# Kernel tuning notes

Hardware: AMD Instinct MI355X
Metric: run time of the kernel (lower is better)

The kernel has to match this reference:

```python
import jax, jax.numpy as jnp
import numpy as np

EPS = 1e-5

def conv(x, w, b=None, padding=0, groups=1, dilation=1):
    out = jax.lax.conv_general_dilated(
        x, w, window_strides=(1, 1), padding=[(padding, padding)] * 2,
        rhs_dilation=(dilation, dilation), feature_group_count=groups,
        dimension_numbers=('NCHW', 'OIHW', 'NCHW'))
    if b is not None:
        out = out + b[None, :, None, None]
    return out

def bn(x, g, b):
    # eval-mode BatchNorm with running_mean=0, running_var=1
    return x * (g / jnp.sqrt(1.0 + EPS))[None, :, None, None] + b[None, :, None, None]

def _gather_bilinear_corner(xf, yi, xi, H, W):
    # xf: [B, C, H*W]; yi/xi: [B, K2, H, W] int32 corner coords
    valid = (yi >= 0) & (yi < H) & (xi >= 0) & (xi < W)
    idx = jnp.clip(yi, 0, H - 1) * W + jnp.clip(xi, 0, W - 1)  # [B,K2,H,W]
    B = xf.shape[0]
    g = jax.vmap(lambda xb, ib: xb[:, ib])(xf, idx.reshape(B, -1))  # [B,C,K2*H*W]
    g = g.reshape(B, xf.shape[1], *yi.shape[1:])  # [B,C,K2,H,W]
    return g * valid[:, None].astype(xf.dtype)

def deform_dw_conv(x, offset, w_dw, pad, dil, kh=3, kw=3):
    # torchvision DeformConv2d, depthwise (groups=C), stride 1.
    # offset: [B, 2*kh*kw, H, W], ordering (dy, dx) per kernel tap.
    B, C, H, W = x.shape
    K2 = kh * kw
    off = offset.reshape(B, K2, 2, H, W)
    dy, dx = off[:, :, 0], off[:, :, 1]  # [B,K2,H,W]
    k = jnp.arange(K2)
    ky = ((k // kw) * dil - pad).astype(x.dtype)  # [K2]
    kx = ((k % kw) * dil - pad).astype(x.dtype)
    py = jnp.arange(H, dtype=x.dtype)[None, None, :, None] + ky[None, :, None, None] + dy
    px = jnp.arange(W, dtype=x.dtype)[None, None, None, :] + kx[None, :, None, None] + dx
    y0 = jnp.floor(py); x0 = jnp.floor(px)
    fy = py - y0; fx = px - x0
    y0i = y0.astype(jnp.int32); x0i = x0.astype(jnp.int32)
    y1i = y0i + 1; x1i = x0i + 1
    xf = x.reshape(B, C, H * W)
    v00 = _gather_bilinear_corner(xf, y0i, x0i, H, W)
    v01 = _gather_bilinear_corner(xf, y0i, x1i, H, W)
    v10 = _gather_bilinear_corner(xf, y1i, x0i, H, W)
    v11 = _gather_bilinear_corner(xf, y1i, x1i, H, W)
    fy = fy[:, None]; fx = fx[:, None]  # [B,1,K2,H,W]
    val = (v00 * (1 - fy) * (1 - fx) + v01 * (1 - fy) * fx
           + v10 * fy * (1 - fx) + v11 * fy * fx)  # [B,C,K2,H,W]
    return jnp.einsum('bckhw,ck->bchw', val, w_dw.reshape(C, K2))

def reference(x, w_conv1, g1, b1, w_off, b_off, w_dw, g_b, b_b,
              w_conv2, g2, b2, w_fc1, b_fc1, w_fc2, b_fc2):
    silu = jax.nn.silu
    h = silu(bn(conv(x, w_conv1), g1, b1))
    # MFC_Bottleneck (n=1): offset conv -> deform depthwise conv -> BN -> SiLU -> residual
    off = conv(h, w_off, b_off, padding=1)
    d = deform_dw_conv(h, off, w_dw, pad=1, dil=1)
    h = silu(bn(d, g_b, b_b)) + h
    y = silu(bn(conv(h, w_conv2), g2, b2))
    # SE block
    s = jnp.mean(y, axis=(2, 3), keepdims=True)
    s = silu(conv(s, w_fc1, b_fc1))
    s = jax.nn.sigmoid(conv(s, w_fc2, b_fc2))
    return y * s

def setup_inputs() -> dict:
    key = jax.random.key(0)
    ks = jax.random.split(key, 8)
    B, C1, C2, HID, H, W = 4, 512, 512, 256, 64, 64
    SQ = C2 // 16
    sc = 0.02
    return {
        'x': jax.random.normal(ks[0], (B, C1, H, W), jnp.float32),
        'w_conv1': jax.random.normal(ks[1], (HID, C1, 1, 1), jnp.float32) * sc,
        'g1': jnp.ones((HID,), jnp.float32),
        'b1': jnp.zeros((HID,), jnp.float32),
        'w_off': jax.random.normal(ks[2], (18, HID, 3, 3), jnp.float32) * sc,
        'b_off': jnp.zeros((18,), jnp.float32),
        'w_dw': jax.random.normal(ks[3], (HID, 1, 3, 3), jnp.float32) * sc,
        'g_b': jnp.ones((HID,), jnp.float32),
        'b_b': jnp.zeros((HID,), jnp.float32),
        'w_conv2': jax.random.normal(ks[4], (C2, HID, 1, 1), jnp.float32) * sc,
        'g2': jnp.ones((C2,), jnp.float32),
        'b2': jnp.zeros((C2,), jnp.float32),
        'w_fc1': jax.random.normal(ks[5], (SQ, C2, 1, 1), jnp.float32) * sc,
        'b_fc1': jnp.zeros((SQ,), jnp.float32),
        'w_fc2': jax.random.normal(ks[6], (C2, SQ, 1, 1), jnp.float32) * sc,
        'b_fc2': jnp.zeros((C2,), jnp.float32),
    }
```

## Files before the change

### kernel.cpp

```cpp
#include <hip/hip_runtime.h>

#define HW 4096
#define BN_RS 0.9999950000374998f

typedef __attribute__((ext_vector_type(8))) short  short8;
typedef __attribute__((ext_vector_type(8))) unsigned short ushort8;
typedef __attribute__((ext_vector_type(4))) float  f32x4;
typedef __attribute__((ext_vector_type(2), aligned(4))) float f32x2u;
typedef __attribute__((ext_vector_type(2), aligned(8))) float f32x2a;

__device__ __forceinline__ float silu_f(float v) { return v / (1.0f + __expf(-v)); }
__device__ __forceinline__ int clamp64(int v) { return v < 0 ? 0 : (v > 63 ? 63 : v); }
__device__ __forceinline__ unsigned short f2bf(float f) {
    union { float f; unsigned u; } v; v.f = f;
    unsigned r = v.u + 0x7fff + ((v.u >> 16) & 1);
    return (unsigned short)(r >> 16);
}
__device__ __forceinline__ unsigned packbf(float lo, float hi) {
    return (unsigned)f2bf(lo) | ((unsigned)f2bf(hi) << 16);
}

template<int CO, int CIN>
__global__ __launch_bounds__(256) void k_conv1x1_mfma(
    const float* __restrict__ X, const float* __restrict__ Wt,
    const float* __restrict__ gg, const float* __restrict__ bb,
    float* __restrict__ Y)
{
    constexpr int NC = CO / 64;
    const int id   = blockIdx.x;
    const int low3 = id & 7;
    const int rest = id >> 3;
    const int c0i  = rest % NC;
    const int tile = (rest / NC) * 8 + low3;
    const int b  = tile >> 6;
    const int p0 = (tile & 63) * 64;
    const int c0 = c0i * 64;

    const int tid  = threadIdx.x;
    const int wave = tid >> 6, lane = tid & 63;
    const int wm = wave >> 1, wn = wave & 1;
    const int lrow = lane & 15, lkg = lane >> 4;

    __shared__ __align__(16) unsigned short As[64 * 40];
    __shared__ __align__(16) unsigned short Bs[64 * 40];

    const float* Xb = X + (size_t)b * CIN * HW;

    f32x4 acc[2][2];
    #pragma unroll
    for (int i = 0; i < 2; ++i)
        #pragma unroll
        for (int j = 0; j < 2; ++j) acc[i][j] = (f32x4){0.f, 0.f, 0.f, 0.f};

    const int arow = tid >> 2, akc = (tid & 3) * 8;
    const int kp = tid >> 4, p4 = (tid & 15) * 4;

    ushort8 aP;
    uint4   bP;

    auto LOAD = [&](int k0) {
        const float* wp = &Wt[(size_t)(c0 + arow) * CIN + k0 + akc];
        float4 v0 = *(const float4*)wp;
        float4 v1 = *(const float4*)(wp + 4);
        ushort8 u;
        u[0] = f2bf(v0.x); u[1] = f2bf(v0.y); u[2] = f2bf(v0.z); u[3] = f2bf(v0.w);
        u[4] = f2bf(v1.x); u[5] = f2bf(v1.y); u[6] = f2bf(v1.z); u[7] = f2bf(v1.w);
        aP = u;
        const float* xp = &Xb[(size_t)(k0 + 2 * kp) * HW + p0 + p4];
        float4 x0 = *(const float4*)xp;
        float4 x1 = *(const float4*)(xp + HW);
        bP.x = packbf(x0.x, x1.x);
        bP.y = packbf(x0.y, x1.y);
        bP.z = packbf(x0.z, x1.z);
        bP.w = packbf(x0.w, x1.w);
    };

    LOAD(0);
    for (int k0 = 0; k0 < CIN; k0 += 32) {
        __syncthreads();
        *(ushort8*)&As[arow * 40 + akc] = aP;
        {
            const int kg = kp >> 2, kl2 = (kp & 3) * 2;
            const unsigned bw[4] = {bP.x, bP.y, bP.z, bP.w};
            #pragma unroll
            for (int jj = 0; jj < 4; ++jj) {
                int pos = p4 + jj;
                int kgs = kg ^ ((pos >> 3) & 3);
                *(unsigned*)&Bs[pos * 40 + kgs * 8 + kl2] = bw[jj];
            }
        }
        __syncthreads();
        if (k0 + 32 < CIN) LOAD(k0 + 32);

        short8 aF[2], bF[2];
        #pragma unroll
        for (int mi = 0; mi < 2; ++mi)
            aF[mi] = *(const short8*)&As[(wm * 32 + mi * 16 + lrow) * 40 + lkg * 8];
        #pragma unroll
        for (int ni = 0; ni < 2; ++ni) {
            int pos = wn * 32 + ni * 16 + lrow;
            int kgs = lkg ^ ((pos >> 3) & 3);
            bF[ni] = *(const short8*)&Bs[pos * 40 + kgs * 8];
        }
        #pragma unroll
        for (int mi = 0; mi < 2; ++mi)
            #pragma unroll
            for (int ni = 0; ni < 2; ++ni)
                acc[mi][ni] = __builtin_amdgcn_mfma_f32_16x16x32_bf16(
                    aF[mi], bF[ni], acc[mi][ni], 0, 0, 0);
    }

    #pragma unroll
    for (int mi = 0; mi < 2; ++mi) {
        #pragma unroll
        for (int r = 0; r < 4; ++r) {
            int co = c0 + wm * 32 + mi * 16 + lkg * 4 + r;
            float s  = gg[co] * BN_RS;
            float bi = bb[co];
            size_t rowb = ((size_t)b * CO + co) * HW + p0 + wn * 32 + lrow;
            Y[rowb]      = silu_f(fmaf(acc[mi][0][r], s, bi));
            Y[rowb + 16] = silu_f(fmaf(acc[mi][1][r], s, bi));
        }
    }
}

__global__ __launch_bounds__(256) void k_woff_t(
    const float* __restrict__ Wo, unsigned short* __restrict__ Wt2)
{
    const int t = blockIdx.x;
    const int co = blockIdx.y;
    const int ci = threadIdx.x;
    float v = (co < 18) ? Wo[((size_t)co * 256 + ci) * 9 + t] : 0.0f;
    Wt2[((size_t)t * 32 + co) * 256 + ci] = f2bf(v);
}

__global__ __launch_bounds__(256) void k_conv_off(
    const float* __restrict__ Hh, const unsigned short* __restrict__ Wt2,
    float* __restrict__ OffP)
{
    const int y = blockIdx.x;
    const int b = blockIdx.y;
    const int q = blockIdx.z;
    const int tid = threadIdx.x;
    const int wn = tid >> 6;
    const int lane = tid & 63;
    const int lrow = lane & 15, lkg = lane >> 4;

    __shared__ __align__(16) unsigned short hsT[3][66][40];

    f32x4 acc[2];
    acc[0] = (f32x4){0.f, 0.f, 0.f, 0.f};
    acc[1] = (f32x4){0.f, 0.f, 0.f, 0.f};

    for (int cc = 0; cc < 2; ++cc) {
        const int ci0 = q * 64 + cc * 32;
        __syncthreads();
        if (tid < 192) {
            int r = tid / 64, which = (tid >> 5) & 1, ci = tid & 31;
            hsT[r][which ? 65 : 0][ci] = 0;
        }
        #pragma unroll
        for (int it = 0; it < 6; ++it) {
            int i  = tid + it * 256;
            int r  = i >> 9;
            int ci = (i >> 4) & 31;
            int x4 = (i & 15) << 2;
            int yy = y + r - 1;
            float4 v = make_float4(0.f, 0.f, 0.f, 0.f);
            if ((unsigned)yy < 64u)
                v = *(const float4*)&Hh[((size_t)(b * 256 + ci0 + ci) << 12) + yy * 64 + x4];
            hsT[r][1 + x4 + 0][ci] = f2bf(v.x);
            hsT[r][1 + x4 + 1][ci] = f2bf(v.y);
            hsT[r][1 + x4 + 2][ci] = f2bf(v.z);
            hsT[r][1 + x4 + 3][ci] = f2bf(v.w);
        }
        __syncthreads();

        #pragma unroll
        for (int t9 = 0; t9 < 9; ++t9) {
            const int ty = t9 / 3, tx = t9 % 3;
            short8 bF = *(const short8*)&hsT[ty][wn * 16 + lrow + tx][lkg * 8];
            #pragma unroll
            for (int mi = 0; mi < 2; ++mi) {
                short8 aF = *(const short8*)&Wt2[((size_t)t9 * 32 + mi * 16 + lrow) * 256
                                                 + ci0 + lkg * 8];
                acc[mi] = __builtin_amdgcn_mfma_f32_16x16x32_bf16(aF, bF, acc[mi], 0, 0, 0);
            }
        }
    }

    #pragma unroll
    for (int mi = 0; mi < 2; ++mi) {
        #pragma unroll
        for (int r = 0; r < 4; ++r) {
            int co = mi * 16 + lkg * 4 + r;
            if (co < 18)
                OffP[(((size_t)q * 4 + b) * 18 + co) * HW + y * 64 + wn * 16 + lrow]
                    = acc[mi][r];
        }
    }
}

__global__ __launch_bounds__(256) void k_off_combine(
    const float* __restrict__ OffP, const float* __restrict__ Bo,
    float* __restrict__ Off2)
{
    const int bk = blockIdx.x;
    const int b = bk / 9, k = bk - b * 9;
    const int t0 = 2 * k, t1 = 2 * k + 1;
    const float bias0 = Bo[t0], bias1 = Bo[t1];
    const size_t p0 = ((size_t)b * 18 + t0) * HW;
    const size_t p1 = ((size_t)b * 18 + t1) * HW;
    float* outp = Off2 + (((size_t)b * 9 + k) * HW) * 2;
    #pragma unroll
    for (int it = 0; it < 4; ++it) {
        int p4 = (threadIdx.x + it * 256) * 4;
        float4 s0 = *(const float4*)&OffP[p0 + p4];
        float4 s1 = *(const float4*)&OffP[p1 + p4];
        #pragma unroll
        for (int q = 1; q < 4; ++q) {
            float4 v0 = *(const float4*)&OffP[((size_t)q * 4 * 18) * HW + p0 + p4];
            float4 v1 = *(const float4*)&OffP[((size_t)q * 4 * 18) * HW + p1 + p4];
            s0.x += v0.x; s0.y += v0.y; s0.z += v0.z; s0.w += v0.w;
            s1.x += v1.x; s1.y += v1.y; s1.z += v1.z; s1.w += v1.w;
        }
        s0.x += bias0; s0.y += bias0; s0.z += bias0; s0.w += bias0;
        s1.x += bias1; s1.y += bias1; s1.z += bias1; s1.w += bias1;
        float4 o01 = make_float4(s0.x, s1.x, s0.y, s1.y);
        float4 o23 = make_float4(s0.z, s1.z, s0.w, s1.w);
        *(float4*)&outp[p4 * 2]     = o01;
        *(float4*)&outp[p4 * 2 + 4] = o23;
    }
}

__global__ __launch_bounds__(256) void k_deform(
    const float* __restrict__ Hh, const float* __restrict__ Off2,
    const float* __restrict__ Wd, const float* __restrict__ Gb,
    const float* __restrict__ Bb, float* __restrict__ H2)
{
    const int idx = blockIdx.x;
    const int bq  = idx & 31;
    const int y   = idx >> 5;
    const int b   = bq >> 3;
    const int q   = bq & 7;
    const int tid = threadIdx.x;
    const int x = tid & 63;
    const int g = tid >> 6;
    const int pos = y * 64 + x;

    __shared__ __align__(16) float hsw[5][32][68];
    __shared__ __align__(16) float wds[9 * 32];
    __shared__ float gbs[32], bbs[32];

    for (int i = tid; i < 288; i += 256) {
        int lc = i & 31, k = i >> 5;
        wds[i] = Wd[(q * 32 + lc) * 9 + k];
    }
    if (tid < 32) {
        gbs[tid] = Gb[q * 32 + tid] * BN_RS;
        bbs[tid] = Bb[q * 32 + tid];
    }

    int w0 = y - 2; w0 = w0 < 0 ? 0 : (w0 > 59 ? 59 : w0);
    const float* hq = Hh + ((size_t)(b * 256 + q * 32) << 12);
    #pragma unroll
    for (int it = 0; it < 10; ++it) {
        int i = tid + it * 256;
        int slot = i >> 9, ch = (i >> 4) & 31, x4 = (i & 15) << 2;
        float4 v = *(const float4*)&hq[((size_t)ch << 12) + (w0 + slot) * 64 + x4];
        *(float4*)&hsw[slot][ch][x4] = v;
    }
    __syncthreads();

    float acc[8];
    #pragma unroll
    for (int j = 0; j < 8; ++j) acc[j] = 0.f;

    const float* Ob   = Off2 + ((size_t)b * 9 * HW + pos) * 2;
    const float* hb0  = hq + ((size_t)(g * 8) << 12);
    const float* ldsb = &hsw[0][0][0];

    for (int r = 0; r < 3; ++r) {
        int   rb0[3], rb1[3], lb0[3], lb1[3];
        float wa0[3], wb0[3], wa1[3], wb1[3];
        bool inw = true;
        #pragma unroll
        for (int t = 0; t < 3; ++t) {
            int k = r * 3 + t;
            f32x2a dv = *(const f32x2a*)(Ob + (size_t)k * HW * 2);
            float dy = dv.x, dx = dv.y;
            float py = (float)(y + r - 1) + dy;
            float px = (float)(x + t - 1) + dx;
            float fy0 = floorf(py), fx0 = floorf(px);
            int y0 = (int)fy0, x0 = (int)fx0;
            float fy = py - fy0, fx = px - fx0;
            bool vy0 = ((unsigned)y0 < 64u), vy1 = ((unsigned)(y0 + 1) < 64u);
            bool vx0 = ((unsigned)x0 < 64u), vx1 = ((unsigned)(x0 + 1) < 64u);
            int cy0 = clamp64(y0), cy1 = clamp64(y0 + 1);
            int bx  = x0 < 0 ? 0 : (x0 > 62 ? 62 : x0);
            int d0 = x0 - bx;
            bool o0 = d0 > 0;
            bool o1 = d0 >= 0;
            rb0[t] = cy0 * 64 + bx;
            rb1[t] = cy1 * 64 + bx;
            lb0[t] = (cy0 - w0) * 2176 + bx;
            lb1[t] = (cy1 - w0) * 2176 + bx;
            inw = inw && (cy0 >= w0) && (cy1 <= w0 + 4);
            float wy0 = vy0 ? (1.0f - fy) : 0.0f;
            float wy1 = vy1 ? fy : 0.0f;
            float wx0 = vx0 ? (1.0f - fx) : 0.0f;
            float wx1 = vx1 ? fx : 0.0f;
            float wa = (o0 ? 0.0f : wx0) + (o1 ? 0.0f : wx1);
            float wb = (o0 ? wx0 : 0.0f) + (o1 ? wx1 : 0.0f);
            wa0[t] = wa * wy0; wb0[t] = wb * wy0;
            wa1[t] = wa * wy1; wb1[t] = wb * wy1;
        }
        if (__all(inw)) {
            #pragma unroll
            for (int j = 0; j < 8; ++j) {
                const int chb = (g * 8 + j) * 68;
                float a = acc[j];
                #pragma unroll
                for (int t = 0; t < 3; ++t) {
                    f32x2u u0 = *(const f32x2u*)(ldsb + lb0[t] + chb);
                    f32x2u u1 = *(const f32x2u*)(ldsb + lb1[t] + chb);
                    float val = u0.x * wa0[t] + u0.y * wb0[t]
                              + u1.x * wa1[t] + u1.y * wb1[t];
                    a = fmaf(val, wds[(r * 3 + t) * 32 + g * 8 + j], a);
                }
                acc[j] = a;
            }
        } else {
            #pragma unroll
            for (int j = 0; j < 8; ++j) {
                const float* hb = hb0 + ((size_t)j << 12);
                float a = acc[j];
                #pragma unroll
                for (int t = 0; t < 3; ++t) {
                    f32x2u u0 = *(const f32x2u*)(hb + rb0[t]);
                    f32x2u u1 = *(const f32x2u*)(hb + rb1[t]);
                    float val = u0.x * wa0[t] + u0.y * wb0[t]
                              + u1.x * wa1[t] + u1.y * wb1[t];
                    a = fmaf(val, wds[(r * 3 + t) * 32 + g * 8 + j], a);
                }
                acc[j] = a;
            }
        }
    }

    const int ry = (y - w0) * 2176 + x;
    #pragma unroll
    for (int j = 0; j < 8; ++j) {
        int lc = g * 8 + j;
        float t = fmaf(acc[j], gbs[lc], bbs[lc]);
        float res = ldsb[ry + lc * 68];
        __builtin_nontemporal_store(silu_f(t) + res,
            &H2[((size_t)(b * 256 + q * 32 + lc) << 12) + pos]);
    }
}

__global__ __launch_bounds__(256) void k_se_reduce(
    const float* __restrict__ Y, float* __restrict__ sb)
{
    const int bc = blockIdx.x;
    const float4* p = (const float4*)(Y + (size_t)bc * HW);
    int tid = threadIdx.x;
    float s = 0.f;
    #pragma unroll
    for (int it = 0; it < 4; ++it) {
        float4 v = p[tid + it * 256];
        s += v.x + v.y + v.z + v.w;
    }
    #pragma unroll
    for (int o = 32; o > 0; o >>= 1) s += __shfl_down(s, o);
    __shared__ float red[4];
    if ((tid & 63) == 0) red[tid >> 6] = s;
    __syncthreads();
    if (tid == 0) sb[bc] = (red[0] + red[1] + red[2] + red[3]) * (1.0f / 4096.0f);
}

__global__ __launch_bounds__(256) void k_se_fc(
    const float* __restrict__ sb, const float* __restrict__ wf1,
    const float* __restrict__ bf1, const float* __restrict__ wf2,
    const float* __restrict__ bf2, float* __restrict__ s2)
{
    const int b = blockIdx.x;
    const int t = threadIdx.x;
    __shared__ float sv[512];
    __shared__ float s1[32];
    sv[t]       = sb[b * 512 + t];
    sv[t + 256] = sb[b * 512 + t + 256];
    __syncthreads();
    if (t < 32) {
        float a = bf1[t];
        const float* w = wf1 + t * 512;
        for (int i = 0; i < 512; ++i) a = fmaf(w[i], sv[i], a);
        s1[t] = silu_f(a);
    }
    __syncthreads();
    #pragma unroll
    for (int it = 0; it < 2; ++it) {
        int co = t + it * 256;
        float a = bf2[co];
        const float* w = wf2 + co * 32;
        #pragma unroll
        for (int i = 0; i < 32; ++i) a = fmaf(w[i], s1[i], a);
        s2[b * 512 + co] = 1.0f / (1.0f + __expf(-a));
    }
}

__global__ __launch_bounds__(256) void k_se_scale(
    float* __restrict__ Y, const float* __restrict__ s2)
{
    size_t i = (size_t)blockIdx.x * 256 + threadIdx.x;
    int bc = (int)(i >> 10);
    float sc = s2[bc];
    float4 v = ((float4*)Y)[i];
    v.x *= sc; v.y *= sc; v.z *= sc; v.w *= sc;
    ((float4*)Y)[i] = v;
}

extern "C" void kernel_launch(void* const* d_in, const int* in_sizes, int n_in,
                              void* d_out, int out_size, void* d_ws, size_t ws_size,
                              hipStream_t stream)
{
    const float* x   = (const float*)d_in[0];
    const float* w1  = (const float*)d_in[1];
    const float* g1  = (const float*)d_in[2];
    const float* b1  = (const float*)d_in[3];
    const float* wof = (const float*)d_in[4];
    const float* bof = (const float*)d_in[5];
    const float* wdw = (const float*)d_in[6];
    const float* gb  = (const float*)d_in[7];
    const float* bbv = (const float*)d_in[8];
    const float* w2  = (const float*)d_in[9];
    const float* g2  = (const float*)d_in[10];
    const float* b2  = (const float*)d_in[11];
    const float* wf1 = (const float*)d_in[12];
    const float* bf1 = (const float*)d_in[13];
    const float* wf2 = (const float*)d_in[14];
    const float* bf2 = (const float*)d_in[15];
    float* out = (float*)d_out;

    const size_t n_h    = 4ull * 256 * HW;
    const size_t n_offp = 4ull * 4 * 18 * HW;
    const size_t n_off  = 4ull * 18 * HW;
    const size_t n_wt2  = 9 * 32 * 256 / 2;
    float* ws = (float*)d_ws;
    float *h, *offp, *offc, *h2, *sb, *s2, *wt2f;
    size_t need = (2 * n_h + n_offp + n_off + 2048 + 2048 + n_wt2 + 1024) * sizeof(float);
    if (ws_size >= need) {
        h = ws; offp = h + n_h; offc = offp + n_offp; h2 = offc + n_off;
        sb = h2 + n_h; s2 = sb + 2048; wt2f = s2 + 2048;
    } else {
        h = out;
        offp = ws; offc = offp + n_offp; h2 = offc + n_off;
        sb = h2 + n_h; s2 = sb + 2048; wt2f = s2 + 2048;
    }
    unsigned short* wt2 = (unsigned short*)wt2f;

    k_conv1x1_mfma<256, 512><<<1024, 256, 0, stream>>>(x, w1, g1, b1, h);
    k_woff_t<<<dim3(9, 32), 256, 0, stream>>>(wof, wt2);
    k_conv_off<<<dim3(64, 4, 4), 256, 0, stream>>>(h, wt2, offp);
    k_off_combine<<<36, 256, 0, stream>>>(offp, bof, offc);
    k_deform<<<2048, 256, 0, stream>>>(h, offc, wdw, gb, bbv, h2);
    k_conv1x1_mfma<512, 256><<<2048, 256, 0, stream>>>(h2, w2, g2, b2, out);
    k_se_reduce<<<2048, 256, 0, stream>>>(out, sb);
    k_se_fc<<<4, 256, 0, stream>>>(sb, wf1, bf1, wf2, bf2, s2);
    k_se_scale<<<8192, 256, 0, stream>>>(out, s2);
}
```

Baseline: 133.7 us.

## Fuse SE average-pool into conv2 epilogue and halve conv1 pixel tile

The second 1x1 conv epilogue now reduces its SiLU outputs per channel across lanes and writes partial sums to a buffer, so the separate SE reduce kernel and its full re-read of the output are removed. The SE FC kernel sums 128 partials per channel itself. The first 1x1 conv also moves to a 32-pixel tile with twice as many blocks, which raises parallelism but halves reuse of the weight tile. The extra shuffles and the serial 128-step partial sum in a 4-block kernel add some cost.

Result: slower. 144.6 us (+8.1%).

```diff
diff --git a/kernel.cpp b/kernel.cpp
--- a/kernel.cpp
+++ b/kernel.cpp
@@ -20,20 +20,24 @@
     return (unsigned)f2bf(lo) | ((unsigned)f2bf(hi) << 16);
 }
 
-template<int CO, int CIN>
+template<int CO, int CIN, int PT, bool SE>
 __global__ __launch_bounds__(256) void k_conv1x1_mfma(
     const float* __restrict__ X, const float* __restrict__ Wt,
     const float* __restrict__ gg, const float* __restrict__ bb,
-    float* __restrict__ Y)
+    float* __restrict__ Y, float* __restrict__ pbuf)
 {
     constexpr int NC = CO / 64;
+    constexpr int PTILES = HW / PT;
+    constexpr int NI = PT / 32;
+
     const int id   = blockIdx.x;
     const int low3 = id & 7;
     const int rest = id >> 3;
     const int c0i  = rest % NC;
     const int tile = (rest / NC) * 8 + low3;
-    const int b  = tile >> 6;
-    const int p0 = (tile & 63) * 64;
+    const int b  = tile / PTILES;
+    const int pt = tile - b * PTILES;
+    const int p0 = pt * PT;
     const int c0 = c0i * 64;
 
     const int tid  = threadIdx.x;
@@ -42,21 +46,22 @@
     const int lrow = lane & 15, lkg = lane >> 4;
 
     __shared__ __align__(16) unsigned short As[64 * 40];
-    __shared__ __align__(16) unsigned short Bs[64 * 40];
+    __shared__ __align__(16) unsigned short Bs[PT * 40];
 
     const float* Xb = X + (size_t)b * CIN * HW;
 
-    f32x4 acc[2][2];
+    f32x4 acc[2][NI];
     #pragma unroll
     for (int i = 0; i < 2; ++i)
         #pragma unroll
-        for (int j = 0; j < 2; ++j) acc[i][j] = (f32x4){0.f, 0.f, 0.f, 0.f};
+        for (int j = 0; j < NI; ++j) acc[i][j] = (f32x4){0.f, 0.f, 0.f, 0.f};
 
     const int arow = tid >> 2, akc = (tid & 3) * 8;
-    const int kp = tid >> 4, p4 = (tid & 15) * 4;
+    const int kp = tid >> 4;
 
     ushort8 aP;
-    uint4   bP;
+    uint4   bP4;
+    uint2   bP2;
 
     auto LOAD = [&](int k0) {
         const float* wp = &Wt[(size_t)(c0 + arow) * CIN + k0 + akc];
@@ -66,13 +71,23 @@
         u[0] = f2bf(v0.x); u[1] = f2bf(v0.y); u[2] = f2bf(v0.z); u[3] = f2bf(v0.w);
         u[4] = f2bf(v1.x); u[5] = f2bf(v1.y); u[6] = f2bf(v1.z); u[7] = f2bf(v1.w);
         aP = u;
-        const float* xp = &Xb[(size_t)(k0 + 2 * kp) * HW + p0 + p4];
-        float4 x0 = *(const float4*)xp;
-        float4 x1 = *(const float4*)(xp + HW);
-        bP.x = packbf(x0.x, x1.x);
-        bP.y = packbf(x0.y, x1.y);
-        bP.z = packbf(x0.z, x1.z);
-        bP.w = packbf(x0.w, x1.w);
+        if constexpr (PT == 64) {
+            const int p4 = (tid & 15) * 4;
+            const float* xp = &Xb[(size_t)(k0 + 2 * kp) * HW + p0 + p4];
+            float4 x0 = *(const float4*)xp;
+            float4 x1 = *(const float4*)(xp + HW);
+            bP4.x = packbf(x0.x, x1.x);
+            bP4.y = packbf(x0.y, x1.y);
+            bP4.z = packbf(x0.z, x1.z);
+            bP4.w = packbf(x0.w, x1.w);
+        } else {
+            const int p2 = (tid & 15) * 2;
+            const float* xp = &Xb[(size_t)(k0 + 2 * kp) * HW + p0 + p2];
+            f32x2a x0 = *(const f32x2a*)xp;
+            f32x2a x1 = *(const f32x2a*)(xp + HW);
+            bP2.x = packbf(x0.x, x1.x);
+            bP2.y = packbf(x0.y, x1.y);
+        }
     };
 
     LOAD(0);
@@ -81,31 +96,43 @@
         *(ushort8*)&As[arow * 40 + akc] = aP;
         {
             const int kg = kp >> 2, kl2 = (kp & 3) * 2;
-            const unsigned bw[4] = {bP.x, bP.y, bP.z, bP.w};
-            #pragma unroll
-            for (int jj = 0; jj < 4; ++jj) {
-                int pos = p4 + jj;
-                int kgs = kg ^ ((pos >> 3) & 3);
-                *(unsigned*)&Bs[pos * 40 + kgs * 8 + kl2] = bw[jj];
+            if constexpr (PT == 64) {
+                const int p4 = (tid & 15) * 4;
+                const unsigned bw[4] = {bP4.x, bP4.y, bP4.z, bP4.w};
+                #pragma unroll
+                for (int jj = 0; jj < 4; ++jj) {
+                    int pos = p4 + jj;
+                    int kgs = kg ^ ((pos >> 3) & 3);
+                    *(unsigned*)&Bs[pos * 40 + kgs * 8 + kl2] = bw[jj];
+                }
+            } else {
+                const int p2 = (tid & 15) * 2;
+                const unsigned bw[2] = {bP2.x, bP2.y};
+                #pragma unroll
+                for (int jj = 0; jj < 2; ++jj) {
+                    int pos = p2 + jj;
+                    int kgs = kg ^ ((pos >> 3) & 3);
+                    *(unsigned*)&Bs[pos * 40 + kgs * 8 + kl2] = bw[jj];
+                }
             }
         }
         __syncthreads();
         if (k0 + 32 < CIN) LOAD(k0 + 32);
 
-        short8 aF[2], bF[2];
+        short8 aF[2], bF[NI];
         #pragma unroll
         for (int mi = 0; mi < 2; ++mi)
             aF[mi] = *(const short8*)&As[(wm * 32 + mi * 16 + lrow) * 40 + lkg * 8];
         #pragma unroll
-        for (int ni = 0; ni < 2; ++ni) {
-            int pos = wn * 32 + ni * 16 + lrow;
+        for (int ni = 0; ni < NI; ++ni) {
+            int pos = wn * (PT / 2) + ni * 16 + lrow;
             int kgs = lkg ^ ((pos >> 3) & 3);
             bF[ni] = *(const short8*)&Bs[pos * 40 + kgs * 8];
         }
         #pragma unroll
         for (int mi = 0; mi < 2; ++mi)
             #pragma unroll
-            for (int ni = 0; ni < 2; ++ni)
+            for (int ni = 0; ni < NI; ++ni)
                 acc[mi][ni] = __builtin_amdgcn_mfma_f32_16x16x32_bf16(
                     aF[mi], bF[ni], acc[mi][ni], 0, 0, 0);
     }
@@ -117,9 +144,22 @@
             int co = c0 + wm * 32 + mi * 16 + lkg * 4 + r;
             float s  = gg[co] * BN_RS;
             float bi = bb[co];
-            size_t rowb = ((size_t)b * CO + co) * HW + p0 + wn * 32 + lrow;
-            Y[rowb]      = silu_f(fmaf(acc[mi][0][r], s, bi));
-            Y[rowb + 16] = silu_f(fmaf(acc[mi][1][r], s, bi));
+            size_t rowb = ((size_t)b * CO + co) * HW + p0 + wn * (PT / 2) + lrow;
+            float vs = 0.f;
+            #pragma unroll
+            for (int ni = 0; ni < NI; ++ni) {
+                float v = silu_f(fmaf(acc[mi][ni][r], s, bi));
+                Y[rowb + ni * 16] = v;
+                vs += v;
+            }
+            if (SE) {
+                vs += __shfl_xor(vs, 1);
+                vs += __shfl_xor(vs, 2);
+                vs += __shfl_xor(vs, 4);
+                vs += __shfl_xor(vs, 8);
+                if (lrow == 0)
+                    pbuf[(size_t)(pt * 2 + wn) * (4 * CO) + b * CO + co] = vs;
+            }
         }
     }
 }
@@ -359,28 +399,8 @@
     }
 }
 
-__global__ __launch_bounds__(256) void k_se_reduce(
-    const float* __restrict__ Y, float* __restrict__ sb)
-{
-    const int bc = blockIdx.x;
-    const float4* p = (const float4*)(Y + (size_t)bc * HW);
-    int tid = threadIdx.x;
-    float s = 0.f;
-    #pragma unroll
-    for (int it = 0; it < 4; ++it) {
-        float4 v = p[tid + it * 256];
-        s += v.x + v.y + v.z + v.w;
-    }
-    #pragma unroll
-    for (int o = 32; o > 0; o >>= 1) s += __shfl_down(s, o);
-    __shared__ float red[4];
-    if ((tid & 63) == 0) red[tid >> 6] = s;
-    __syncthreads();
-    if (tid == 0) sb[bc] = (red[0] + red[1] + red[2] + red[3]) * (1.0f / 4096.0f);
-}
-
 __global__ __launch_bounds__(256) void k_se_fc(
-    const float* __restrict__ sb, const float* __restrict__ wf1,
+    const float* __restrict__ pbuf, const float* __restrict__ wf1,
     const float* __restrict__ bf1, const float* __restrict__ wf2,
     const float* __restrict__ bf2, float* __restrict__ s2)
 {
@@ -388,8 +408,14 @@
     const int t = threadIdx.x;
     __shared__ float sv[512];
     __shared__ float s1[32];
-    sv[t]       = sb[b * 512 + t];
-    sv[t + 256] = sb[b * 512 + t + 256];
+    float a0 = 0.f, a1 = 0.f;
+    for (int s = 0; s < 128; ++s) {
+        const float* p = pbuf + (size_t)s * 2048 + b * 512;
+        a0 += p[t];
+        a1 += p[t + 256];
+    }
+    sv[t]       = a0 * (1.0f / 4096.0f);
+    sv[t + 256] = a1 * (1.0f / 4096.0f);
     __syncthreads();
     if (t < 32) {
         float a = bf1[t];
@@ -445,27 +471,27 @@
     const size_t n_h    = 4ull * 256 * HW;
     const size_t n_offp = 4ull * 4 * 18 * HW;
     const size_t n_off  = 4ull * 18 * HW;
+    const size_t n_pb   = 128ull * 4 * 512;
     const size_t n_wt2  = 9 * 32 * 256 / 2;
     float* ws = (float*)d_ws;
-    float *h, *offp, *offc, *h2, *sb, *s2, *wt2f;
-    size_t need = (2 * n_h + n_offp + n_off + 2048 + 2048 + n_wt2 + 1024) * sizeof(float);
+    float *h, *offp, *offc, *h2, *pb, *s2, *wt2f;
+    size_t need = (2 * n_h + n_offp + n_off + n_pb + 2048 + n_wt2 + 1024) * sizeof(float);
     if (ws_size >= need) {
         h = ws; offp = h + n_h; offc = offp + n_offp; h2 = offc + n_off;
-        sb = h2 + n_h; s2 = sb + 2048; wt2f = s2 + 2048;
+        pb = h2 + n_h; s2 = pb + n_pb; wt2f = s2 + 2048;
     } else {
         h = out;
         offp = ws; offc = offp + n_offp; h2 = offc + n_off;
-        sb = h2 + n_h; s2 = sb + 2048; wt2f = s2 + 2048;
+        pb = h2 + n_h; s2 = pb + n_pb; wt2f = s2 + 2048;
     }
     unsigned short* wt2 = (unsigned short*)wt2f;
 
-    k_conv1x1_mfma<256, 512><<<1024, 256, 0, stream>>>(x, w1, g1, b1, h);
+    k_conv1x1_mfma<256, 512, 32, false><<<2048, 256, 0, stream>>>(x, w1, g1, b1, h, nullptr);
     k_woff_t<<<dim3(9, 32), 256, 0, stream>>>(wof, wt2);
     k_conv_off<<<dim3(64, 4, 4), 256, 0, stream>>>(h, wt2, offp);
     k_off_combine<<<36, 256, 0, stream>>>(offp, bof, offc);
     k_deform<<<2048, 256, 0, stream>>>(h, offc, wdw, gb, bbv, h2);
-    k_conv1x1_mfma<512, 256><<<2048, 256, 0, stream>>>(h2, w2, g2, b2, out);
-    k_se_reduce<<<2048, 256, 0, stream>>>(out, sb);
-    k_se_fc<<<4, 256, 0, stream>>>(sb, wf1, bf1, wf2, bf2, s2);
+    k_conv1x1_mfma<512, 256, 64, true><<<2048, 256, 0, stream>>>(h2, w2, g2, b2, out, pb);
+    k_se_fc<<<4, 256, 0, stream>>>(pb, wf1, bf1, wf2, bf2, s2);
     k_se_scale<<<8192, 256, 0, stream>>>(out, s2);
 }
```

## Pre-transpose input to bf16 pixel-major and feed conv1 MFMA directly from global

Applied to the files above, without the earlier changes.

Adds a kernel that converts the input x to bf16 in a pixel-major (transposed) layout and another that converts conv1 weights to bf16. A new conv1 kernel then loads MFMA operands straight from global memory as contiguous 8-element vectors, with no LDS staging. The aim is to remove the conversion and transpose work from the GEMM inner loop. The cost is an extra pass over the 32 MB input (read fp32, write bf16), two more launches, and extra workspace.

New measurement: 160.7 us. +20.2%, slower.

```diff
diff --git a/kernel.cpp b/kernel.cpp
--- a/kernel.cpp
+++ b/kernel.cpp
@@ -5,6 +5,7 @@
 
 typedef __attribute__((ext_vector_type(8))) short  short8;
 typedef __attribute__((ext_vector_type(8))) unsigned short ushort8;
+typedef __attribute__((ext_vector_type(4))) unsigned short ushort4v;
 typedef __attribute__((ext_vector_type(4))) float  f32x4;
 typedef __attribute__((ext_vector_type(2), aligned(4))) float f32x2u;
 typedef __attribute__((ext_vector_type(2), aligned(8))) float f32x2a;
@@ -18,6 +19,103 @@
 }
 __device__ __forceinline__ unsigned packbf(float lo, float hi) {
     return (unsigned)f2bf(lo) | ((unsigned)f2bf(hi) << 16);
+}
+
+__global__ __launch_bounds__(256) void k_xt(
+    const float* __restrict__ X, unsigned short* __restrict__ Xt)
+{
+    const int p0  = blockIdx.x * 64;
+    const int ci0 = blockIdx.y * 64;
+    const int b   = blockIdx.z;
+    const int tid = threadIdx.x;
+    __shared__ float ld[64][65];
+    #pragma unroll
+    for (int it = 0; it < 4; ++it) {
+        int i = tid + it * 256;
+        int ci = i >> 4, c4 = (i & 15) * 4;
+        float4 v = *(const float4*)&X[((size_t)(b * 512 + ci0 + ci) << 12) + p0 + c4];
+        ld[ci][c4] = v.x; ld[ci][c4 + 1] = v.y; ld[ci][c4 + 2] = v.z; ld[ci][c4 + 3] = v.w;
+    }
+    __syncthreads();
+    #pragma unroll
+    for (int it = 0; it < 4; ++it) {
+        int i = tid + it * 256;
+        int pr = i >> 4, oc4 = (i & 15) * 4;
+        ushort4v u;
+        u[0] = f2bf(ld[oc4 + 0][pr]);
+        u[1] = f2bf(ld[oc4 + 1][pr]);
+        u[2] = f2bf(ld[oc4 + 2][pr]);
+        u[3] = f2bf(ld[oc4 + 3][pr]);
+        *(ushort4v*)&Xt[((size_t)(b << 12) + p0 + pr) * 512 + ci0 + oc4] = u;
+    }
+}
+
+__global__ __launch_bounds__(256) void k_w1b(
+    const float* __restrict__ W, unsigned short* __restrict__ Wb)
+{
+    size_t i = ((size_t)blockIdx.x * 256 + threadIdx.x) * 4;
+    float4 v = *(const float4*)&W[i];
+    ushort4v u;
+    u[0] = f2bf(v.x); u[1] = f2bf(v.y); u[2] = f2bf(v.z); u[3] = f2bf(v.w);
+    *(ushort4v*)&Wb[i] = u;
+}
+
+template<int CO, int CIN>
+__global__ __launch_bounds__(256) void k_conv1_td(
+    const unsigned short* __restrict__ Xt, const unsigned short* __restrict__ Wb,
+    const float* __restrict__ gg, const float* __restrict__ bb,
+    float* __restrict__ Y)
+{
+    constexpr int NC = CO / 64;
+    const int id   = blockIdx.x;
+    const int low3 = id & 7;
+    const int rest = id >> 3;
+    const int c0i  = rest % NC;
+    const int tile = (rest / NC) * 8 + low3;
+    const int b  = tile >> 6;
+    const int p0 = (tile & 63) * 64;
+    const int c0 = c0i * 64;
+
+    const int tid  = threadIdx.x;
+    const int wave = tid >> 6, lane = tid & 63;
+    const int wm = wave >> 1, wn = wave & 1;
+    const int lrow = lane & 15, lkg = lane >> 4;
+
+    f32x4 acc[2][2];
+    #pragma unroll
+    for (int i = 0; i < 2; ++i)
+        #pragma unroll
+        for (int j = 0; j < 2; ++j) acc[i][j] = (f32x4){0.f, 0.f, 0.f, 0.f};
+
+    const unsigned short* ap0 = Wb + (size_t)(c0 + wm * 32 + lrow) * CIN + lkg * 8;
+    const unsigned short* ap1 = ap0 + 16 * CIN;
+    const unsigned short* bp0 = Xt + ((size_t)(b << 12) + p0 + wn * 32 + lrow) * CIN + lkg * 8;
+    const unsigned short* bp1 = bp0 + 16 * CIN;
+
+    #pragma unroll 4
+    for (int k0 = 0; k0 < CIN; k0 += 32) {
+        short8 a0 = *(const short8*)(ap0 + k0);
+        short8 a1 = *(const short8*)(ap1 + k0);
+        short8 b0 = *(const short8*)(bp0 + k0);
+        short8 b1 = *(const short8*)(bp1 + k0);
+        acc[0][0] = __builtin_amdgcn_mfma_f32_16x16x32_bf16(a0, b0, acc[0][0], 0, 0, 0);
+        acc[0][1] = __builtin_amdgcn_mfma_f32_16x16x32_bf16(a0, b1, acc[0][1], 0, 0, 0);
+        acc[1][0] = __builtin_amdgcn_mfma_f32_16x16x32_bf16(a1, b0, acc[1][0], 0, 0, 0);
+        acc[1][1] = __builtin_amdgcn_mfma_f32_16x16x32_bf16(a1, b1, acc[1][1], 0, 0, 0);
+    }
+
+    #pragma unroll
+    for (int mi = 0; mi < 2; ++mi) {
+        #pragma unroll
+        for (int r = 0; r < 4; ++r) {
+            int co = c0 + wm * 32 + mi * 16 + lkg * 4 + r;
+            float s  = gg[co] * BN_RS;
+            float bi = bb[co];
+            size_t rowb = ((size_t)b * CO + co) * HW + p0 + wn * 32 + lrow;
+            Y[rowb]      = silu_f(fmaf(acc[mi][0][r], s, bi));
+            Y[rowb + 16] = silu_f(fmaf(acc[mi][1][r], s, bi));
+        }
+    }
 }
 
 template<int CO, int CIN>
@@ -446,20 +544,29 @@
     const size_t n_offp = 4ull * 4 * 18 * HW;
     const size_t n_off  = 4ull * 18 * HW;
     const size_t n_wt2  = 9 * 32 * 256 / 2;
+    const size_t n_xt   = 4ull * HW * 512 / 2;
+    const size_t n_w1b  = 256 * 512 / 2;
     float* ws = (float*)d_ws;
-    float *h, *offp, *offc, *h2, *sb, *s2, *wt2f;
-    size_t need = (2 * n_h + n_offp + n_off + 2048 + 2048 + n_wt2 + 1024) * sizeof(float);
+    float *h, *offp, *offc, *h2, *sb, *s2, *wt2f, *xtf, *w1bf;
+    size_t need = (2 * n_h + n_offp + n_off + 2048 + 2048 + n_wt2 + n_xt + n_w1b + 1024)
+                  * sizeof(float);
     if (ws_size >= need) {
         h = ws; offp = h + n_h; offc = offp + n_offp; h2 = offc + n_off;
         sb = h2 + n_h; s2 = sb + 2048; wt2f = s2 + 2048;
+        xtf = wt2f + n_wt2; w1bf = xtf + n_xt;
     } else {
         h = out;
         offp = ws; offc = offp + n_offp; h2 = offc + n_off;
         sb = h2 + n_h; s2 = sb + 2048; wt2f = s2 + 2048;
+        xtf = wt2f + n_wt2; w1bf = xtf + n_xt;
     }
     unsigned short* wt2 = (unsigned short*)wt2f;
-
-    k_conv1x1_mfma<256, 512><<<1024, 256, 0, stream>>>(x, w1, g1, b1, h);
+    unsigned short* xt  = (unsigned short*)xtf;
+    unsigned short* w1b = (unsigned short*)w1bf;
+
+    k_xt<<<dim3(64, 8, 4), 256, 0, stream>>>(x, xt);
+    k_w1b<<<128, 256, 0, stream>>>(w1, w1b);
+    k_conv1_td<256, 512><<<1024, 256, 0, stream>>>(xt, w1b, g1, b1, h);
     k_woff_t<<<dim3(9, 32), 256, 0, stream>>>(wof, wt2);
     k_conv_off<<<dim3(64, 4, 4), 256, 0, stream>>>(h, wt2, offp);
     k_off_combine<<<36, 256, 0, stream>>>(offp, bof, offc);
```
